# Kernel optimization log

Measured on AMD Instinct MI355X. Metric: run time of the kernel, lower is better.

## Reference

```python
import jax, jax.numpy as jnp
import numpy as np


def setup_inputs() -> dict:
    key = jax.random.key(0)
    k1, k2, k3, k4 = jax.random.split(key, 4)
    B, S, IN, H = 4, 2048, 512, 1024
    x = jax.random.normal(k1, (B, S, IN), dtype=jnp.float32)
    W1 = jax.random.normal(k2, (IN, H), dtype=jnp.float32) * (1.0 / np.sqrt(IN))
    b1 = jax.random.normal(k3, (H,), dtype=jnp.float32) * 0.02
    Wq = jax.random.normal(k4, (H, H), dtype=jnp.float32) * (1.0 / np.sqrt(H))
    return {"x": x, "W1": W1, "b1": b1, "Wq": Wq, "atten_size": 16}


def reference(x, W1, b1, Wq, atten_size):
    A = atten_size
    B, S, _ = x.shape
    H = W1.shape[1]
    h = jax.nn.relu(jnp.einsum('bsi,ih->bsh', x, W1) + b1)  # [B,S,H]
    # zero-pad sequence dim by A on each side
    padded = jnp.pad(h, ((0, 0), (A, A), (0, 0)))  # [B,S+2A,H]
    # torch: stack(roll(padded, k, 1) for k in -A..A, dim=2) then slice [A:-A]
    # => x_nei[b, i, j] = padded[b, 2A + i - j]
    idx = 2 * A + jnp.arange(S)[:, None] - jnp.arange(2 * A + 1)[None, :]  # [S,W]
    x_nei = padded[:, idx, :]  # [B,S,W,H]
    q = jnp.einsum('bsh,hk->bsk', h, Wq)  # [B,S,H]
    scores = jnp.einsum('bsh,bswh->bsw', q, x_nei) / jnp.sqrt(jnp.asarray(H, x.dtype))
    w = jax.nn.softmax(scores, axis=2)  # softmax over window axis
    out = jnp.einsum('bsw,bswh->bsh', w, x_nei)
    return out
```

## Files before the change

kernel.cpp:

```cpp
#include <hip/hip_runtime.h>
#include <stdint.h>

constexpr int BATCH = 4;
constexpr int SEQ   = 2048;
constexpr int DIN   = 512;
constexpr int DH    = 1024;
constexpr int BS    = BATCH * SEQ;
constexpr int AP    = 32;
constexpr int AW    = 64;

typedef float  floatx4 __attribute__((ext_vector_type(4)));
typedef short  bf16x8  __attribute__((ext_vector_type(8)));

static __device__ __forceinline__ unsigned short f2bf(float f) {
  union { float f; unsigned u; } v; v.f = f;
  unsigned r = (v.u + 0x7fffu + ((v.u >> 16) & 1u)) >> 16;
  return (unsigned short)r;
}

static __device__ __forceinline__ void gld_lds16(const unsigned short* g, const short* l) {
  typedef const __attribute__((address_space(1))) void* gvp;
  typedef __attribute__((address_space(3))) void* lvp;
  __builtin_amdgcn_global_load_lds((gvp)(uintptr_t)g, (lvp)(unsigned)(uintptr_t)l, 16, 0, 0);
}

__global__ __launch_bounds__(256) void prep_k(const float* __restrict__ X,
                                              const float* __restrict__ W1,
                                              const float* __restrict__ Wq,
                                              unsigned short* __restrict__ Xb,
                                              unsigned short* __restrict__ w1t,
                                              unsigned short* __restrict__ wqt) {
  __shared__ float t[32][33];
  if (blockIdx.y >= 48) {
    const int t0 = ((blockIdx.y - 48) * 32 + blockIdx.x) * 256 + threadIdx.x;
    const float4 a = ((const float4*)X)[(size_t)t0 * 2];
    const float4 b = ((const float4*)X)[(size_t)t0 * 2 + 1];
    __align__(16) unsigned short o[8];
    o[0] = f2bf(a.x); o[1] = f2bf(a.y); o[2] = f2bf(a.z); o[3] = f2bf(a.w);
    o[4] = f2bf(b.x); o[5] = f2bf(b.y); o[6] = f2bf(b.z); o[7] = f2bf(b.w);
    *(uint4*)(Xb + (size_t)t0 * 8) = *(const uint4*)o;
    return;
  }
  const bool isW1 = blockIdx.y < 16;
  const float* in = isW1 ? W1 : Wq;
  unsigned short* out = isW1 ? w1t : wqt;
  const int R = isW1 ? DIN : DH;
  const int C = DH;
  const int r0 = (isW1 ? blockIdx.y : (blockIdx.y - 16)) * 32;
  const int c0 = blockIdx.x * 32;
  const int tx = threadIdx.x & 31, ty = threadIdx.x >> 5;
  for (int i = ty; i < 32; i += 8) t[i][tx] = in[(size_t)(r0 + i) * C + c0 + tx];
  __syncthreads();
  for (int i = ty; i < 32; i += 8) out[(size_t)(c0 + i) * R + r0 + tx] = f2bf(t[tx][i]);
}

__global__ __launch_bounds__(256) void gemm1_k(const unsigned short* __restrict__ Ab,
                                               const unsigned short* __restrict__ Bt,
                                               const float* __restrict__ bias,
                                               unsigned short* __restrict__ outB,
                                               unsigned short* __restrict__ outBT) {
  const int M = BS, N = DH, K = DIN;
  __shared__ __align__(16) short As0[128 * 32], As1[128 * 32];
  __shared__ __align__(16) short Bs0[128 * 32], Bs1[128 * 32];
  const int tid  = threadIdx.x;
  const int m0   = blockIdx.x * 128, n0 = blockIdx.y * 128;
  const int wv   = tid >> 6, lane = tid & 63;
  const int wm   = (wv >> 1) * 64, wn = (wv & 1) * 64;
  const int l16  = lane & 15, quad = lane >> 4;

  const int ra = lane >> 2, ca = (lane & 3) * 8;
  const unsigned short* gA = Ab + (size_t)(m0 + wv * 32 + ra) * K + ca;
  const unsigned short* gB = Bt + (size_t)(n0 + wv * 32 + ra) * K + ca;
  const short* lA0a = &As0[wv * 1024];
  const short* lA0b = &As0[wv * 1024 + 512];
  const short* lA1a = &As1[wv * 1024];
  const short* lA1b = &As1[wv * 1024 + 512];
  const short* lB0a = &Bs0[wv * 1024];
  const short* lB0b = &Bs0[wv * 1024 + 512];
  const short* lB1a = &Bs1[wv * 1024];
  const short* lB1b = &Bs1[wv * 1024 + 512];

  floatx4 acc[4][4];
  for (int i = 0; i < 4; i++)
    for (int j = 0; j < 4; j++) acc[i][j] = {0.f, 0.f, 0.f, 0.f};

  for (int ks = 0; ks < K / 64; ++ks) {
    __syncthreads();
    gld_lds16(gA, lA0a); gld_lds16(gA + 16 * K, lA0b);
    gld_lds16(gA + 32, lA1a); gld_lds16(gA + 16 * K + 32, lA1b);
    gld_lds16(gB, lB0a); gld_lds16(gB + 16 * K, lB0b);
    gld_lds16(gB + 32, lB1a); gld_lds16(gB + 16 * K + 32, lB1b);
    gA += 64; gB += 64;
    __syncthreads();
    bf16x8 af[4], bfr[4];
    for (int i = 0; i < 4; i++)
      af[i] = *(const bf16x8*)&As0[(wm + i * 16 + l16) * 32 + quad * 8];
    for (int j = 0; j < 4; j++)
      bfr[j] = *(const bf16x8*)&Bs0[(wn + j * 16 + l16) * 32 + quad * 8];
    for (int i = 0; i < 4; i++)
      for (int j = 0; j < 4; j++)
        acc[i][j] = __builtin_amdgcn_mfma_f32_16x16x32_bf16(af[i], bfr[j], acc[i][j], 0, 0, 0);
    for (int i = 0; i < 4; i++)
      af[i] = *(const bf16x8*)&As1[(wm + i * 16 + l16) * 32 + quad * 8];
    for (int j = 0; j < 4; j++)
      bfr[j] = *(const bf16x8*)&Bs1[(wn + j * 16 + l16) * 32 + quad * 8];
    for (int i = 0; i < 4; i++)
      for (int j = 0; j < 4; j++)
        acc[i][j] = __builtin_amdgcn_mfma_f32_16x16x32_bf16(af[i], bfr[j], acc[i][j], 0, 0, 0);
  }

  for (int j = 0; j < 4; j++) {
    const int col = n0 + wn + j * 16 + l16;
    const float bv = bias[col];
    for (int i = 0; i < 4; i++) {
      const int rowb = m0 + wm + i * 16 + quad * 4;
      float v[4];
      for (int r = 0; r < 4; r++) v[r] = fmaxf(acc[i][j][r] + bv, 0.f);
      for (int r = 0; r < 4; r++) outB[(size_t)(rowb + r) * N + col] = f2bf(v[r]);
      ushort4 o4; o4.x = f2bf(v[0]); o4.y = f2bf(v[1]); o4.z = f2bf(v[2]); o4.w = f2bf(v[3]);
      *(ushort4*)(outBT + (size_t)col * M + rowb) = o4;
    }
  }
}

__global__ __launch_bounds__(256) void gemm2_k(const unsigned short* __restrict__ Ab,
                                               const unsigned short* __restrict__ Bt,
                                               unsigned short* __restrict__ outB) {
  const int N = DH, K = DH;
  __shared__ __align__(16) short As0[128 * 32], As1[128 * 32];
  __shared__ __align__(16) short Bs0[128 * 32], Bs1[128 * 32];
  const int tid  = threadIdx.x;
  const int m0   = blockIdx.x * 128, n0 = blockIdx.y * 128;
  const int wv   = tid >> 6, lane = tid & 63;
  const int wm   = (wv >> 1) * 64, wn = (wv & 1) * 64;
  const int l16  = lane & 15, quad = lane >> 4;

  const int ra = lane >> 2, ca = (lane & 3) * 8;
  const unsigned short* gA = Ab + (size_t)(m0 + wv * 32 + ra) * K + ca;
  const unsigned short* gB = Bt + (size_t)(n0 + wv * 32 + ra) * K + ca;
  const short* lA0a = &As0[wv * 1024];
  const short* lA0b = &As0[wv * 1024 + 512];
  const short* lA1a = &As1[wv * 1024];
  const short* lA1b = &As1[wv * 1024 + 512];
  const short* lB0a = &Bs0[wv * 1024];
  const short* lB0b = &Bs0[wv * 1024 + 512];
  const short* lB1a = &Bs1[wv * 1024];
  const short* lB1b = &Bs1[wv * 1024 + 512];

  floatx4 acc[4][4];
  for (int i = 0; i < 4; i++)
    for (int j = 0; j < 4; j++) acc[i][j] = {0.f, 0.f, 0.f, 0.f};

  for (int ks = 0; ks < K / 64; ++ks) {
    __syncthreads();
    gld_lds16(gA, lA0a); gld_lds16(gA + 16 * K, lA0b);
    gld_lds16(gA + 32, lA1a); gld_lds16(gA + 16 * K + 32, lA1b);
    gld_lds16(gB, lB0a); gld_lds16(gB + 16 * K, lB0b);
    gld_lds16(gB + 32, lB1a); gld_lds16(gB + 16 * K + 32, lB1b);
    gA += 64; gB += 64;
    __syncthreads();
    bf16x8 af[4], bfr[4];
    for (int i = 0; i < 4; i++)
      af[i] = *(const bf16x8*)&As0[(wm + i * 16 + l16) * 32 + quad * 8];
    for (int j = 0; j < 4; j++)
      bfr[j] = *(const bf16x8*)&Bs0[(wn + j * 16 + l16) * 32 + quad * 8];
    for (int i = 0; i < 4; i++)
      for (int j = 0; j < 4; j++)
        acc[i][j] = __builtin_amdgcn_mfma_f32_16x16x32_bf16(af[i], bfr[j], acc[i][j], 0, 0, 0);
    for (int i = 0; i < 4; i++)
      af[i] = *(const bf16x8*)&As1[(wm + i * 16 + l16) * 32 + quad * 8];
    for (int j = 0; j < 4; j++)
      bfr[j] = *(const bf16x8*)&Bs1[(wn + j * 16 + l16) * 32 + quad * 8];
    for (int i = 0; i < 4; i++)
      for (int j = 0; j < 4; j++)
        acc[i][j] = __builtin_amdgcn_mfma_f32_16x16x32_bf16(af[i], bfr[j], acc[i][j], 0, 0, 0);
  }

  for (int j = 0; j < 4; j++) {
    const int col = n0 + wn + j * 16 + l16;
    for (int i = 0; i < 4; i++) {
      const int rowb = m0 + wm + i * 16 + quad * 4;
      for (int r = 0; r < 4; r++)
        outB[(size_t)(rowb + r) * N + col] = f2bf(acc[i][j][r]);
    }
  }
}

__global__ __launch_bounds__(1024) void attn_mfma_k(const unsigned short* __restrict__ hb,
                                                    const unsigned short* __restrict__ hbT,
                                                    const unsigned short* __restrict__ qb,
                                                    float* __restrict__ out) {
  __shared__ float Sf[2][32 * 64];
  __shared__ __align__(16) short Ps[32 * 72];

  const int tid  = threadIdx.x;
  const int wave = tid >> 6, lane = tid & 63;
  const int l16  = lane & 15, quad = lane >> 4;
  const int p0   = blockIdx.x * AP;
  const int s0   = p0 & (SEQ - 1);

  if (tid < 32 * 72 / 2) ((unsigned*)Ps)[tid] = 0;
  else if (tid < 32 * 72 / 2 + 128) ((unsigned*)Ps)[tid] = (tid - 1024 < 32 * 72 / 2 - 1024) ? 0u : 0u;
  if (tid >= 1024 - 128 && tid - (1024 - 128) + 1024 < 1152) ((unsigned*)Ps)[tid - (1024 - 128) + 1024] = 0;

  {
    const int kh = wave & 1;
    const int nt = (wave >> 1) & 3;
    const int mt = wave >> 3;
    const unsigned short* qp = qb + (size_t)(p0 + mt * 16 + l16) * DH + kh * 512 + quad * 8;
    const int hrow = s0 - 16 + nt * 16 + l16;
    const bool hv = (hrow >= 0) && (hrow < SEQ);
    const unsigned short* hp = hb + (long long)(p0 - 16 + nt * 16 + l16) * DH + kh * 512 + quad * 8;

    floatx4 ac[4] = {{0,0,0,0},{0,0,0,0},{0,0,0,0},{0,0,0,0}};
    const bf16x8 hz = {0,0,0,0,0,0,0,0};
    __builtin_amdgcn_s_setprio(1);
    #pragma unroll
    for (int it = 0; it < 16; ++it) {
      bf16x8 qa = *(const bf16x8*)(qp + it * 32);
      bf16x8 ha = hz;
      if (hv) ha = *(const bf16x8*)(hp + it * 32);
      ac[it & 3] = __builtin_amdgcn_mfma_f32_16x16x32_bf16(qa, ha, ac[it & 3], 0, 0, 0);
    }
    __builtin_amdgcn_s_setprio(0);
    floatx4 s4;
    for (int r = 0; r < 4; r++)
      s4[r] = (ac[0][r] + ac[1][r]) + (ac[2][r] + ac[3][r]);
    for (int r = 0; r < 4; r++)
      Sf[kh][(mt * 16 + quad * 4 + r) * 64 + nt * 16 + l16] = s4[r] * (1.f / 32.f);
  }
  __syncthreads();

  if (tid < 512) {
    const int row = tid >> 4, k = tid & 15;
    const float v0 = Sf[0][row * 64 + row + k] + Sf[1][row * 64 + row + k];
    const float v1 = Sf[0][row * 64 + row + k + 16] + Sf[1][row * 64 + row + k + 16];
    const float v2 = (k == 0) ? (Sf[0][row * 64 + row + 32] + Sf[1][row * 64 + row + 32]) : -1e30f;
    float mx = fmaxf(v0, fmaxf(v1, v2));
    for (int off = 1; off < 16; off <<= 1) mx = fmaxf(mx, __shfl_xor(mx, off, 64));
    const float e0 = __expf(v0 - mx), e1 = __expf(v1 - mx);
    const float e2 = (k == 0) ? __expf(v2 - mx) : 0.f;
    float sum = e0 + e1 + e2;
    for (int off = 1; off < 16; off <<= 1) sum += __shfl_xor(sum, off, 64);
    const float inv = 1.f / sum;
    Ps[row * 72 + row + k] = f2bf(e0 * inv);
    Ps[row * 72 + row + k + 16] = f2bf(e1 * inv);
    if (k == 0) Ps[row * 72 + row + 32] = f2bf(e2 * inv);
  }
  __syncthreads();

  {
    const bf16x8 pb00 = *(const bf16x8*)&Ps[(l16) * 72 + quad * 8];
    const bf16x8 pb01 = *(const bf16x8*)&Ps[(l16) * 72 + 32 + quad * 8];
    const bf16x8 pb10 = *(const bf16x8*)&Ps[(16 + l16) * 72 + quad * 8];
    const bf16x8 pb11 = *(const bf16x8*)&Ps[(16 + l16) * 72 + 32 + quad * 8];

    int lo = 16 - s0; if (lo < 0) lo = 0;
    int hi = SEQ + 16 - s0; if (hi > AW) hi = AW;
    const bool interior = (lo == 0) && (hi == AW);

    #pragma unroll
    for (int i = 0; i < 4; ++i) {
      const int mt2 = wave * 4 + i;
      const unsigned short* ap = hbT + (size_t)(mt2 * 16 + l16) * BS + (p0 - 16) + quad * 8;
      bf16x8 aa0 = *(const bf16x8*)(ap);
      bf16x8 aa1 = *(const bf16x8*)(ap + 32);
      if (!interior) {
        #pragma unroll
        for (int j = 0; j < 8; j++) {
          const int k = quad * 8 + j;
          if (k < lo || k >= hi) aa0[j] = 0;
          if (k + 32 < lo || k + 32 >= hi) aa1[j] = 0;
        }
      }
      floatx4 o0 = {0.f, 0.f, 0.f, 0.f}, o1 = {0.f, 0.f, 0.f, 0.f};
      __builtin_amdgcn_s_setprio(1);
      o0 = __builtin_amdgcn_mfma_f32_16x16x32_bf16(aa0, pb00, o0, 0, 0, 0);
      o0 = __builtin_amdgcn_mfma_f32_16x16x32_bf16(aa1, pb01, o0, 0, 0, 0);
      o1 = __builtin_amdgcn_mfma_f32_16x16x32_bf16(aa0, pb10, o1, 0, 0, 0);
      o1 = __builtin_amdgcn_mfma_f32_16x16x32_bf16(aa1, pb11, o1, 0, 0, 0);
      __builtin_amdgcn_s_setprio(0);
      float4 s0v; s0v.x = o0[0]; s0v.y = o0[1]; s0v.z = o0[2]; s0v.w = o0[3];
      float4 s1v; s1v.x = o1[0]; s1v.y = o1[1]; s1v.z = o1[2]; s1v.w = o1[3];
      *(float4*)(out + (size_t)(p0 + l16) * DH + mt2 * 16 + quad * 4) = s0v;
      *(float4*)(out + (size_t)(p0 + 16 + l16) * DH + mt2 * 16 + quad * 4) = s1v;
    }
  }
}

extern "C" void kernel_launch(void* const* d_in, const int* in_sizes, int n_in,
                              void* d_out, int out_size, void* d_ws, size_t ws_size,
                              hipStream_t stream) {
  const float* x  = (const float*)d_in[0];
  const float* W1 = (const float*)d_in[1];
  const float* b1 = (const float*)d_in[2];
  const float* Wq = (const float*)d_in[3];

  char* w = (char*)d_ws;
  unsigned short* w1t = (unsigned short*)(w);
  unsigned short* wqt = (unsigned short*)(w + (1ull  << 20));
  unsigned short* hb  = (unsigned short*)(w + (3ull  << 20));
  unsigned short* hbT = (unsigned short*)(w + (19ull << 20));
  unsigned short* qb  = (unsigned short*)(w + (35ull << 20));
  unsigned short* xb  = qb;

  prep_k<<<dim3(32, 112), 256, 0, stream>>>(x, W1, Wq, xb, w1t, wqt);

  gemm1_k<<<dim3(BS / 128, DH / 128), 256, 0, stream>>>(xb, w1t, b1, hb, hbT);
  gemm2_k<<<dim3(BS / 128, DH / 128), 256, 0, stream>>>(hb, wqt, qb);

  attn_mfma_k<<<BS / AP, 1024, 0, stream>>>(hb, hbT, qb, (float*)d_out);
}
```

Baseline: 158.5 us.

## Fuse Q projection GEMM into attention kernel via LDS-staged h tile

```diff
diff --git a/kernel.cpp b/kernel.cpp
--- a/kernel.cpp
+++ b/kernel.cpp
@@ -123,73 +123,11 @@
   }
 }
 
-__global__ __launch_bounds__(256) void gemm2_k(const unsigned short* __restrict__ Ab,
-                                               const unsigned short* __restrict__ Bt,
-                                               unsigned short* __restrict__ outB) {
-  const int N = DH, K = DH;
-  __shared__ __align__(16) short As0[128 * 32], As1[128 * 32];
-  __shared__ __align__(16) short Bs0[128 * 32], Bs1[128 * 32];
-  const int tid  = threadIdx.x;
-  const int m0   = blockIdx.x * 128, n0 = blockIdx.y * 128;
-  const int wv   = tid >> 6, lane = tid & 63;
-  const int wm   = (wv >> 1) * 64, wn = (wv & 1) * 64;
-  const int l16  = lane & 15, quad = lane >> 4;
-
-  const int ra = lane >> 2, ca = (lane & 3) * 8;
-  const unsigned short* gA = Ab + (size_t)(m0 + wv * 32 + ra) * K + ca;
-  const unsigned short* gB = Bt + (size_t)(n0 + wv * 32 + ra) * K + ca;
-  const short* lA0a = &As0[wv * 1024];
-  const short* lA0b = &As0[wv * 1024 + 512];
-  const short* lA1a = &As1[wv * 1024];
-  const short* lA1b = &As1[wv * 1024 + 512];
-  const short* lB0a = &Bs0[wv * 1024];
-  const short* lB0b = &Bs0[wv * 1024 + 512];
-  const short* lB1a = &Bs1[wv * 1024];
-  const short* lB1b = &Bs1[wv * 1024 + 512];
-
-  floatx4 acc[4][4];
-  for (int i = 0; i < 4; i++)
-    for (int j = 0; j < 4; j++) acc[i][j] = {0.f, 0.f, 0.f, 0.f};
-
-  for (int ks = 0; ks < K / 64; ++ks) {
-    __syncthreads();
-    gld_lds16(gA, lA0a); gld_lds16(gA + 16 * K, lA0b);
-    gld_lds16(gA + 32, lA1a); gld_lds16(gA + 16 * K + 32, lA1b);
-    gld_lds16(gB, lB0a); gld_lds16(gB + 16 * K, lB0b);
-    gld_lds16(gB + 32, lB1a); gld_lds16(gB + 16 * K + 32, lB1b);
-    gA += 64; gB += 64;
-    __syncthreads();
-    bf16x8 af[4], bfr[4];
-    for (int i = 0; i < 4; i++)
-      af[i] = *(const bf16x8*)&As0[(wm + i * 16 + l16) * 32 + quad * 8];
-    for (int j = 0; j < 4; j++)
-      bfr[j] = *(const bf16x8*)&Bs0[(wn + j * 16 + l16) * 32 + quad * 8];
-    for (int i = 0; i < 4; i++)
-      for (int j = 0; j < 4; j++)
-        acc[i][j] = __builtin_amdgcn_mfma_f32_16x16x32_bf16(af[i], bfr[j], acc[i][j], 0, 0, 0);
-    for (int i = 0; i < 4; i++)
-      af[i] = *(const bf16x8*)&As1[(wm + i * 16 + l16) * 32 + quad * 8];
-    for (int j = 0; j < 4; j++)
-      bfr[j] = *(const bf16x8*)&Bs1[(wn + j * 16 + l16) * 32 + quad * 8];
-    for (int i = 0; i < 4; i++)
-      for (int j = 0; j < 4; j++)
-        acc[i][j] = __builtin_amdgcn_mfma_f32_16x16x32_bf16(af[i], bfr[j], acc[i][j], 0, 0, 0);
-  }
-
-  for (int j = 0; j < 4; j++) {
-    const int col = n0 + wn + j * 16 + l16;
-    for (int i = 0; i < 4; i++) {
-      const int rowb = m0 + wm + i * 16 + quad * 4;
-      for (int r = 0; r < 4; r++)
-        outB[(size_t)(rowb + r) * N + col] = f2bf(acc[i][j][r]);
-    }
-  }
-}
-
-__global__ __launch_bounds__(1024) void attn_mfma_k(const unsigned short* __restrict__ hb,
-                                                    const unsigned short* __restrict__ hbT,
-                                                    const unsigned short* __restrict__ qb,
-                                                    float* __restrict__ out) {
+__global__ __launch_bounds__(1024, 4) void attn_fused_k(const unsigned short* __restrict__ hb,
+                                                        const unsigned short* __restrict__ hbT,
+                                                        const unsigned short* __restrict__ wqt,
+                                                        float* __restrict__ out) {
+  __shared__ __align__(16) unsigned short Hq[32 * 1024];
   __shared__ float Sf[2][32 * 64];
   __shared__ __align__(16) short Ps[32 * 72];
 
@@ -199,15 +137,60 @@
   const int p0   = blockIdx.x * AP;
   const int s0   = p0 & (SEQ - 1);
 
-  if (tid < 32 * 72 / 2) ((unsigned*)Ps)[tid] = 0;
-  else if (tid < 32 * 72 / 2 + 128) ((unsigned*)Ps)[tid] = (tid - 1024 < 32 * 72 / 2 - 1024) ? 0u : 0u;
-  if (tid >= 1024 - 128 && tid - (1024 - 128) + 1024 < 1152) ((unsigned*)Ps)[tid - (1024 - 128) + 1024] = 0;
+  for (int i = tid; i < 32 * 72 / 2; i += 1024) ((unsigned*)Ps)[i] = 0;
+
+  {
+    const int r  = tid >> 5;
+    const int c0 = (tid & 31) * 32;
+    const unsigned short* src = hb + (size_t)(p0 + r) * DH + c0;
+    #pragma unroll
+    for (int c = 0; c < 4; c++) {
+      uint4 v = *(const uint4*)(src + c * 8);
+      const int colu = (c0 + c * 8) ^ ((r & 15) << 3);
+      *(uint4*)&Hq[r * 1024 + colu] = v;
+    }
+  }
+  __syncthreads();
+
+  floatx4 qa[2][4];
+  {
+    for (int i = 0; i < 2; i++)
+      for (int j = 0; j < 4; j++) qa[i][j] = {0.f, 0.f, 0.f, 0.f};
+    const int wcol = wave * 64;
+    const unsigned short* gq = wqt + (size_t)(wcol + l16) * DH + quad * 8;
+    #pragma unroll 2
+    for (int it = 0; it < 32; ++it) {
+      const int cb = it * 32 + quad * 8;
+      const int sw = cb ^ (l16 << 3);
+      bf16x8 a0 = *(const bf16x8*)&Hq[l16 * 1024 + sw];
+      bf16x8 a1 = *(const bf16x8*)&Hq[(16 + l16) * 1024 + sw];
+      #pragma unroll
+      for (int j = 0; j < 4; j++) {
+        bf16x8 b = *(const bf16x8*)(gq + (size_t)(j * 16) * DH + it * 32);
+        qa[0][j] = __builtin_amdgcn_mfma_f32_16x16x32_bf16(a0, b, qa[0][j], 0, 0, 0);
+        qa[1][j] = __builtin_amdgcn_mfma_f32_16x16x32_bf16(a1, b, qa[1][j], 0, 0, 0);
+      }
+    }
+  }
+  __syncthreads();
+
+  {
+    const int wcol = wave * 64;
+    for (int i = 0; i < 2; i++)
+      for (int j = 0; j < 4; j++)
+        for (int r = 0; r < 4; r++) {
+          const int row  = i * 16 + quad * 4 + r;
+          const int colu = wcol + j * 16 + l16;
+          Hq[row * 1024 + (colu ^ ((row & 15) << 3))] = f2bf(qa[i][j][r]);
+        }
+  }
+  __syncthreads();
 
   {
     const int kh = wave & 1;
     const int nt = (wave >> 1) & 3;
     const int mt = wave >> 3;
-    const unsigned short* qp = qb + (size_t)(p0 + mt * 16 + l16) * DH + kh * 512 + quad * 8;
+    const int qrow = mt * 16 + l16;
     const int hrow = s0 - 16 + nt * 16 + l16;
     const bool hv = (hrow >= 0) && (hrow < SEQ);
     const unsigned short* hp = hb + (long long)(p0 - 16 + nt * 16 + l16) * DH + kh * 512 + quad * 8;
@@ -217,10 +200,11 @@
     __builtin_amdgcn_s_setprio(1);
     #pragma unroll
     for (int it = 0; it < 16; ++it) {
-      bf16x8 qa = *(const bf16x8*)(qp + it * 32);
+      const int cb = kh * 512 + it * 32 + quad * 8;
+      bf16x8 qf = *(const bf16x8*)&Hq[qrow * 1024 + (cb ^ (l16 << 3))];
       bf16x8 ha = hz;
       if (hv) ha = *(const bf16x8*)(hp + it * 32);
-      ac[it & 3] = __builtin_amdgcn_mfma_f32_16x16x32_bf16(qa, ha, ac[it & 3], 0, 0, 0);
+      ac[it & 3] = __builtin_amdgcn_mfma_f32_16x16x32_bf16(qf, ha, ac[it & 3], 0, 0, 0);
     }
     __builtin_amdgcn_s_setprio(0);
     floatx4 s4;
@@ -301,13 +285,11 @@
   unsigned short* wqt = (unsigned short*)(w + (1ull  << 20));
   unsigned short* hb  = (unsigned short*)(w + (3ull  << 20));
   unsigned short* hbT = (unsigned short*)(w + (19ull << 20));
-  unsigned short* qb  = (unsigned short*)(w + (35ull << 20));
-  unsigned short* xb  = qb;
+  unsigned short* xb  = (unsigned short*)(w + (35ull << 20));
 
   prep_k<<<dim3(32, 112), 256, 0, stream>>>(x, W1, Wq, xb, w1t, wqt);
 
   gemm1_k<<<dim3(BS / 128, DH / 128), 256, 0, stream>>>(xb, w1t, b1, hb, hbT);
-  gemm2_k<<<dim3(BS / 128, DH / 128), 256, 0, stream>>>(hb, wqt, qb);
-
-  attn_mfma_k<<<BS / AP, 1024, 0, stream>>>(hb, hbT, qb, (float*)d_out);
-}
+
+  attn_fused_k<<<BS / AP, 1024, 0, stream>>>(hb, hbT, wqt, (float*)d_out);
+}
```

Result: slower. 186.6 us (+17.8%).

## Double-buffer LDS in both GEMM kernels to prefetch the next K slice

Applied to the files above, without the earlier changes.

```diff
diff --git a/kernel.cpp b/kernel.cpp
--- a/kernel.cpp
+++ b/kernel.cpp
@@ -60,53 +60,60 @@
                                                unsigned short* __restrict__ outB,
                                                unsigned short* __restrict__ outBT) {
   const int M = BS, N = DH, K = DIN;
-  __shared__ __align__(16) short As0[128 * 32], As1[128 * 32];
-  __shared__ __align__(16) short Bs0[128 * 32], Bs1[128 * 32];
+  __shared__ __align__(16) short As[2][2 * 128 * 32];
+  __shared__ __align__(16) short Bs[2][2 * 128 * 32];
   const int tid  = threadIdx.x;
   const int m0   = blockIdx.x * 128, n0 = blockIdx.y * 128;
   const int wv   = tid >> 6, lane = tid & 63;
   const int wm   = (wv >> 1) * 64, wn = (wv & 1) * 64;
   const int l16  = lane & 15, quad = lane >> 4;
-
-  const int ra = lane >> 2, ca = (lane & 3) * 8;
+  const int ra   = lane >> 2, ca = (lane & 3) * 8;
+
   const unsigned short* gA = Ab + (size_t)(m0 + wv * 32 + ra) * K + ca;
   const unsigned short* gB = Bt + (size_t)(n0 + wv * 32 + ra) * K + ca;
-  const short* lA0a = &As0[wv * 1024];
-  const short* lA0b = &As0[wv * 1024 + 512];
-  const short* lA1a = &As1[wv * 1024];
-  const short* lA1b = &As1[wv * 1024 + 512];
-  const short* lB0a = &Bs0[wv * 1024];
-  const short* lB0b = &Bs0[wv * 1024 + 512];
-  const short* lB1a = &Bs1[wv * 1024];
-  const short* lB1b = &Bs1[wv * 1024 + 512];
 
   floatx4 acc[4][4];
   for (int i = 0; i < 4; i++)
     for (int j = 0; j < 4; j++) acc[i][j] = {0.f, 0.f, 0.f, 0.f};
 
-  for (int ks = 0; ks < K / 64; ++ks) {
+  auto stage = [&](int buf, int koff) {
+    const unsigned short* a = gA + koff;
+    const unsigned short* b = gB + koff;
+    short* la = &As[buf][wv * 1024];
+    gld_lds16(a, la);
+    gld_lds16(a + 16 * K, la + 512);
+    gld_lds16(a + 32, la + 4096);
+    gld_lds16(a + 16 * K + 32, la + 4096 + 512);
+    short* lb = &Bs[buf][wv * 1024];
+    gld_lds16(b, lb);
+    gld_lds16(b + 16 * K, lb + 512);
+    gld_lds16(b + 32, lb + 4096);
+    gld_lds16(b + 16 * K + 32, lb + 4096 + 512);
+  };
+
+  stage(0, 0);
+  __syncthreads();
+  const int NK = K / 64;
+  for (int ks = 0; ks < NK; ++ks) {
+    const int cur = ks & 1;
+    if (ks + 1 < NK) stage(cur ^ 1, (ks + 1) * 64);
+    const short* Ac = As[cur];
+    const short* Bc = Bs[cur];
+    bf16x8 af[4], bfr[4];
+    #pragma unroll
+    for (int h = 0; h < 2; h++) {
+      const int ho = h * 4096;
+      for (int i = 0; i < 4; i++)
+        af[i] = *(const bf16x8*)&Ac[ho + (wm + i * 16 + l16) * 32 + quad * 8];
+      for (int j = 0; j < 4; j++)
+        bfr[j] = *(const bf16x8*)&Bc[ho + (wn + j * 16 + l16) * 32 + quad * 8];
+      __builtin_amdgcn_s_setprio(1);
+      for (int i = 0; i < 4; i++)
+        for (int j = 0; j < 4; j++)
+          acc[i][j] = __builtin_amdgcn_mfma_f32_16x16x32_bf16(af[i], bfr[j], acc[i][j], 0, 0, 0);
+      __builtin_amdgcn_s_setprio(0);
+    }
     __syncthreads();
-    gld_lds16(gA, lA0a); gld_lds16(gA + 16 * K, lA0b);
-    gld_lds16(gA + 32, lA1a); gld_lds16(gA + 16 * K + 32, lA1b);
-    gld_lds16(gB, lB0a); gld_lds16(gB + 16 * K, lB0b);
-    gld_lds16(gB + 32, lB1a); gld_lds16(gB + 16 * K + 32, lB1b);
-    gA += 64; gB += 64;
-    __syncthreads();
-    bf16x8 af[4], bfr[4];
-    for (int i = 0; i < 4; i++)
-      af[i] = *(const bf16x8*)&As0[(wm + i * 16 + l16) * 32 + quad * 8];
-    for (int j = 0; j < 4; j++)
-      bfr[j] = *(const bf16x8*)&Bs0[(wn + j * 16 + l16) * 32 + quad * 8];
-    for (int i = 0; i < 4; i++)
-      for (int j = 0; j < 4; j++)
-        acc[i][j] = __builtin_amdgcn_mfma_f32_16x16x32_bf16(af[i], bfr[j], acc[i][j], 0, 0, 0);
-    for (int i = 0; i < 4; i++)
-      af[i] = *(const bf16x8*)&As1[(wm + i * 16 + l16) * 32 + quad * 8];
-    for (int j = 0; j < 4; j++)
-      bfr[j] = *(const bf16x8*)&Bs1[(wn + j * 16 + l16) * 32 + quad * 8];
-    for (int i = 0; i < 4; i++)
-      for (int j = 0; j < 4; j++)
-        acc[i][j] = __builtin_amdgcn_mfma_f32_16x16x32_bf16(af[i], bfr[j], acc[i][j], 0, 0, 0);
   }
 
   for (int j = 0; j < 4; j++) {
@@ -127,53 +134,60 @@
                                                const unsigned short* __restrict__ Bt,
                                                unsigned short* __restrict__ outB) {
   const int N = DH, K = DH;
-  __shared__ __align__(16) short As0[128 * 32], As1[128 * 32];
-  __shared__ __align__(16) short Bs0[128 * 32], Bs1[128 * 32];
+  __shared__ __align__(16) short As[2][2 * 128 * 32];
+  __shared__ __align__(16) short Bs[2][2 * 128 * 32];
   const int tid  = threadIdx.x;
   const int m0   = blockIdx.x * 128, n0 = blockIdx.y * 128;
   const int wv   = tid >> 6, lane = tid & 63;
   const int wm   = (wv >> 1) * 64, wn = (wv & 1) * 64;
   const int l16  = lane & 15, quad = lane >> 4;
-
-  const int ra = lane >> 2, ca = (lane & 3) * 8;
+  const int ra   = lane >> 2, ca = (lane & 3) * 8;
+
   const unsigned short* gA = Ab + (size_t)(m0 + wv * 32 + ra) * K + ca;
   const unsigned short* gB = Bt + (size_t)(n0 + wv * 32 + ra) * K + ca;
-  const short* lA0a = &As0[wv * 1024];
-  const short* lA0b = &As0[wv * 1024 + 512];
-  const short* lA1a = &As1[wv * 1024];
-  const short* lA1b = &As1[wv * 1024 + 512];
-  const short* lB0a = &Bs0[wv * 1024];
-  const short* lB0b = &Bs0[wv * 1024 + 512];
-  const short* lB1a = &Bs1[wv * 1024];
-  const short* lB1b = &Bs1[wv * 1024 + 512];
 
   floatx4 acc[4][4];
   for (int i = 0; i < 4; i++)
     for (int j = 0; j < 4; j++) acc[i][j] = {0.f, 0.f, 0.f, 0.f};
 
-  for (int ks = 0; ks < K / 64; ++ks) {
+  auto stage = [&](int buf, int koff) {
+    const unsigned short* a = gA + koff;
+    const unsigned short* b = gB + koff;
+    short* la = &As[buf][wv * 1024];
+    gld_lds16(a, la);
+    gld_lds16(a + 16 * K, la + 512);
+    gld_lds16(a + 32, la + 4096);
+    gld_lds16(a + 16 * K + 32, la + 4096 + 512);
+    short* lb = &Bs[buf][wv * 1024];
+    gld_lds16(b, lb);
+    gld_lds16(b + 16 * K, lb + 512);
+    gld_lds16(b + 32, lb + 4096);
+    gld_lds16(b + 16 * K + 32, lb + 4096 + 512);
+  };
+
+  stage(0, 0);
+  __syncthreads();
+  const int NK = K / 64;
+  for (int ks = 0; ks < NK; ++ks) {
+    const int cur = ks & 1;
+    if (ks + 1 < NK) stage(cur ^ 1, (ks + 1) * 64);
+    const short* Ac = As[cur];
+    const short* Bc = Bs[cur];
+    bf16x8 af[4], bfr[4];
+    #pragma unroll
+    for (int h = 0; h < 2; h++) {
+      const int ho = h * 4096;
+      for (int i = 0; i < 4; i++)
+        af[i] = *(const bf16x8*)&Ac[ho + (wm + i * 16 + l16) * 32 + quad * 8];
+      for (int j = 0; j < 4; j++)
+        bfr[j] = *(const bf16x8*)&Bc[ho + (wn + j * 16 + l16) * 32 + quad * 8];
+      __builtin_amdgcn_s_setprio(1);
+      for (int i = 0; i < 4; i++)
+        for (int j = 0; j < 4; j++)
+          acc[i][j] = __builtin_amdgcn_mfma_f32_16x16x32_bf16(af[i], bfr[j], acc[i][j], 0, 0, 0);
+      __builtin_amdgcn_s_setprio(0);
+    }
     __syncthreads();
-    gld_lds16(gA, lA0a); gld_lds16(gA + 16 * K, lA0b);
-    gld_lds16(gA + 32, lA1a); gld_lds16(gA + 16 * K + 32, lA1b);
-    gld_lds16(gB, lB0a); gld_lds16(gB + 16 * K, lB0b);
-    gld_lds16(gB + 32, lB1a); gld_lds16(gB + 16 * K + 32, lB1b);
-    gA += 64; gB += 64;
-    __syncthreads();
-    bf16x8 af[4], bfr[4];
-    for (int i = 0; i < 4; i++)
-      af[i] = *(const bf16x8*)&As0[(wm + i * 16 + l16) * 32 + quad * 8];
-    for (int j = 0; j < 4; j++)
-      bfr[j] = *(const bf16x8*)&Bs0[(wn + j * 16 + l16) * 32 + quad * 8];
-    for (int i = 0; i < 4; i++)
-      for (int j = 0; j < 4; j++)
-        acc[i][j] = __builtin_amdgcn_mfma_f32_16x16x32_bf16(af[i], bfr[j], acc[i][j], 0, 0, 0);
-    for (int i = 0; i < 4; i++)
-      af[i] = *(const bf16x8*)&As1[(wm + i * 16 + l16) * 32 + quad * 8];
-    for (int j = 0; j < 4; j++)
-      bfr[j] = *(const bf16x8*)&Bs1[(wn + j * 16 + l16) * 32 + quad * 8];
-    for (int i = 0; i < 4; i++)
-      for (int j = 0; j < 4; j++)
-        acc[i][j] = __builtin_amdgcn_mfma_f32_16x16x32_bf16(af[i], bfr[j], acc[i][j], 0, 0, 0);
   }
 
   for (int j = 0; j < 4; j++) {
@@ -199,9 +213,7 @@
   const int p0   = blockIdx.x * AP;
   const int s0   = p0 & (SEQ - 1);
 
-  if (tid < 32 * 72 / 2) ((unsigned*)Ps)[tid] = 0;
-  else if (tid < 32 * 72 / 2 + 128) ((unsigned*)Ps)[tid] = (tid - 1024 < 32 * 72 / 2 - 1024) ? 0u : 0u;
-  if (tid >= 1024 - 128 && tid - (1024 - 128) + 1024 < 1152) ((unsigned*)Ps)[tid - (1024 - 128) + 1024] = 0;
+  for (int i = tid; i < 32 * 72 / 2; i += 1024) ((unsigned*)Ps)[i] = 0;
 
   {
     const int kh = wave & 1;
```

After: 155.1 us. 1.02x faster.
